# Kernel optimization log

Measured on AMD Instinct MI355X. Metric: run time of the kernel, lower is better.

The kernel has to match this reference:

```python
import jax, jax.numpy as jnp
import numpy as np


def _conv1d_same(seq, w, b):
    # seq: (N, 1, C), w: (1, 1, K) odd K, bias (1,). SAME padding, stride 1.
    k = w.shape[-1]
    p = (k - 1) // 2
    out = jax.lax.conv_general_dilated(
        seq, w, window_strides=(1,), padding=[(p, p)],
        dimension_numbers=("NCH", "OIH", "NCH"))
    return out + b[None, :, None]


def setup_inputs() -> dict:
    key = jax.random.key(0)
    k1, k2, k3 = jax.random.split(key, 3)
    N, C, H, W = 32, 512, 32, 32
    x = jax.random.normal(k1, (N, C, H, W), dtype=jnp.float32)
    wq = jax.random.normal(k2, (1, 1, 5), dtype=jnp.float32) * 0.2
    bq = jax.random.normal(k3, (1,), dtype=jnp.float32) * 0.1
    return {"x": x, "wq": wq, "bq": bq}


def reference(x, wq, bq):
    N, C, H, W = x.shape
    # Global average pool over spatial dims -> (N, 1, C)
    gap = jnp.mean(x, axis=(2, 3)).reshape(N, 1, C)
    # NOTE: original module applies conv_q to BOTH query and key (conv_k unused)
    query = jax.nn.sigmoid(_conv1d_same(gap, wq, bq))          # (N, 1, C)
    key_t = jnp.transpose(query, (0, 2, 1))                    # (N, C, 1)
    # Outer product key @ query -> (N, C, C), softmax over flattened C*C
    qk = jnp.einsum("nci,nij->ncj", key_t, query)              # (N, C, C)
    qk = jax.nn.softmax(qk.reshape(N, C * C), axis=-1).reshape(N, C, C)
    # value: (N, H*W, C)
    value = jnp.transpose(x, (0, 2, 3, 1)).reshape(N, H * W, C)
    att = jnp.einsum("npc,ncd->npd", value, qk)                # (N, HW, C)
    att = jnp.transpose(att, (0, 2, 1)).reshape(N, C, H, W)
    return x * att
```

## Files before the change

kernel.cpp:

```cpp
#include <hip/hip_runtime.h>
#include <math.h>

#define NB 32
#define CC 512
#define HW 1024
#define NJ 10

typedef float vf4 __attribute__((ext_vector_type(4)));

__device__ float g_gap[NB * CC];
__device__ float g_q[NB * CC];
__device__ float g_invZ[NB];

__device__ __forceinline__ float wave_reduce(float s) {
#pragma unroll
  for (int off = 32; off; off >>= 1) s += __shfl_down(s, off, 64);
  return s;
}

__global__ __launch_bounds__(256) void k_gap(const float* __restrict__ x) {
  int wv = threadIdx.x >> 6, lane = threadIdx.x & 63;
  int r0 = blockIdx.x * 16;
#pragma unroll
  for (int it = 0; it < 4; ++it) {
    int row = r0 + wv * 4 + it;
    const float4* xp = (const float4*)x + (size_t)row * 256;
    float s = 0.f;
#pragma unroll
    for (int k = 0; k < 4; ++k) {
      float4 v = xp[lane + 64 * k];
      s += v.x + v.y + v.z + v.w;
    }
    s = wave_reduce(s);
    if (lane == 0) g_gap[row] = s * (1.0f / 1024.0f);
  }
}

__global__ __launch_bounds__(512) void k_q(const float* __restrict__ wq,
                                           const float* __restrict__ bq) {
  int n = blockIdx.x, c = threadIdx.x;
  int wv = c >> 6, lane = c & 63;
  __shared__ float gsh[CC];
  __shared__ float wred[8][NJ];
  const float cj[NJ] = {1.f, 1.f, 0.5f, 1.f / 6.f, 1.f / 24.f, 1.f / 120.f,
                        1.f / 720.f, 1.f / 5040.f, 1.f / 40320.f, 1.f / 362880.f};
  gsh[c] = g_gap[n * CC + c];
  __syncthreads();
  float z = bq[0];
#pragma unroll
  for (int k = 0; k < 5; ++k) {
    int idx = c + k - 2;
    float gv = (idx >= 0 && idx < CC) ? gsh[idx] : 0.f;
    z = fmaf(gv, wq[k], z);
  }
  float qv = 1.f / (1.f + expf(-z));
  g_q[n * CC + c] = qv;
  float pj[NJ];
  float pw = 1.f;
#pragma unroll
  for (int j = 0; j < NJ; ++j) { pj[j] = pw; pw *= qv; }
#pragma unroll
  for (int j = 0; j < NJ; ++j) pj[j] = wave_reduce(pj[j]);
  if (lane == 0) {
#pragma unroll
    for (int j = 0; j < NJ; ++j) wred[wv][j] = pj[j];
  }
  __syncthreads();
  if (c == 0) {
    float Z = 0.f;
#pragma unroll
    for (int j = 0; j < NJ; ++j) {
      float P = 0.f;
#pragma unroll
      for (int w8 = 0; w8 < 8; ++w8) P += wred[w8][j];
      Z = fmaf(cj[j] * P, P, Z);
    }
    g_invZ[n] = 1.f / Z;
  }
}

__global__ __launch_bounds__(512, 2) void k_fused(const float* __restrict__ x,
                                                  float* __restrict__ out) {
  int n = blockIdx.x >> 5, pblk = blockIdx.x & 31;
  int t = threadIdx.x;
  int cg = t >> 3, pg = t & 7;
  int wv = t >> 6, lane = t & 63;

  __shared__ vf4 sred[8][8][NJ + 1];
  __shared__ vf4 sfin[8][NJ + 1];

  const float cj[NJ] = {1.f, 1.f, 0.5f, 1.f / 6.f, 1.f / 24.f, 1.f / 120.f,
                        1.f / 720.f, 1.f / 5040.f, 1.f / 40320.f, 1.f / 362880.f};

  const vf4* x4 = (const vf4*)x;
  size_t base = (size_t)(n * CC + cg * 8) * 256 + (size_t)pblk * 8 + pg;

  vf4 xv[8];
#pragma unroll
  for (int i = 0; i < 8; ++i)
    xv[i] = __builtin_nontemporal_load(&x4[base + (size_t)i * 256]);

  float qv8[8];
  {
    const vf4* q4 = (const vf4*)g_q;
    int qi = (n * CC + cg * 8) >> 2;
    vf4 qa = q4[qi], qb = q4[qi + 1];
    qv8[0] = qa.x; qv8[1] = qa.y; qv8[2] = qa.z; qv8[3] = qa.w;
    qv8[4] = qb.x; qv8[5] = qb.y; qv8[6] = qb.z; qv8[7] = qb.w;
  }
  float invZ = g_invZ[n];

  vf4 acc[NJ];
#pragma unroll
  for (int j = 0; j < NJ; ++j) acc[j] = (vf4){0.f, 0.f, 0.f, 0.f};
#pragma unroll
  for (int i = 0; i < 8; ++i) {
    float qc = qv8[i];
    vf4 v = xv[i];
    float w = 1.f;
#pragma unroll
    for (int j = 0; j < NJ; ++j) {
      acc[j] += v * w;
      w *= qc;
    }
  }
#pragma unroll
  for (int j = 0; j < NJ; ++j) {
#pragma unroll
    for (int m = 8; m <= 32; m <<= 1) {
      acc[j].x += __shfl_xor(acc[j].x, m, 64);
      acc[j].y += __shfl_xor(acc[j].y, m, 64);
      acc[j].z += __shfl_xor(acc[j].z, m, 64);
      acc[j].w += __shfl_xor(acc[j].w, m, 64);
    }
  }
  if (lane < 8) {
#pragma unroll
    for (int j = 0; j < NJ; ++j) sred[wv][lane][j] = acc[j];
  }
  __syncthreads();
  if (t < 80) {
    int pp = t / NJ, j = t - pp * NJ;
    vf4 a = (vf4){0.f, 0.f, 0.f, 0.f};
#pragma unroll
    for (int w8 = 0; w8 < 8; ++w8) a += sred[w8][pp][j];
    sfin[pp][j] = a * (cj[j] * invZ);
  }
  __syncthreads();

  vf4 sj[NJ];
#pragma unroll
  for (int j = 0; j < NJ; ++j) sj[j] = sfin[pg][j];
  vf4* o4 = (vf4*)out;
#pragma unroll
  for (int i = 0; i < 8; ++i) {
    float qd = qv8[i];
    float w = 1.f;
    vf4 att = (vf4){0.f, 0.f, 0.f, 0.f};
#pragma unroll
    for (int j = 0; j < NJ; ++j) {
      att += sj[j] * w;
      w *= qd;
    }
    __builtin_nontemporal_store(xv[i] * att, &o4[base + (size_t)i * 256]);
  }
}

extern "C" void kernel_launch(void* const* d_in, const int* in_sizes, int n_in,
                              void* d_out, int out_size, void* d_ws, size_t ws_size,
                              hipStream_t stream) {
  const float* x  = (const float*)d_in[0];
  const float* wq = (const float*)d_in[1];
  const float* bq = (const float*)d_in[2];
  float* out = (float*)d_out;
  (void)d_ws; (void)ws_size;

  k_gap<<<NB * CC / 16, 256, 0, stream>>>(x);
  k_q<<<NB, 512, 0, stream>>>(wq, bq);
  k_fused<<<NB * 32, 512, 0, stream>>>(x, out);
}
```

Baseline: 143.0 us.

## Widen fused tile to 16 channels by 16 pixel-groups, stage q in shared memory

The fused kernel now has each thread cover 16 channels and each block 64 pixels, which halves the grid to 512 blocks. Per-channel q values are staged in LDS, and the 10-term power accumulation is split into two halves of 5 to limit live registers. Nontemporal loads and stores are swapped for ordinary ones. Each thread now holds 16 x values and the grid is smaller, so register pressure rises and occupancy and parallelism may fall.

Measured after the change: 127.8 us. 1.12x faster.

```diff
diff --git a/kernel.cpp b/kernel.cpp
--- a/kernel.cpp
+++ b/kernel.cpp
@@ -81,65 +81,70 @@
 
 __global__ __launch_bounds__(512, 2) void k_fused(const float* __restrict__ x,
                                                   float* __restrict__ out) {
-  int n = blockIdx.x >> 5, pblk = blockIdx.x & 31;
+  int n = blockIdx.x >> 4, pblk = blockIdx.x & 15;
   int t = threadIdx.x;
-  int cg = t >> 3, pg = t & 7;
+  int cg = t >> 4, pg = t & 15;
   int wv = t >> 6, lane = t & 63;
 
-  __shared__ vf4 sred[8][8][NJ + 1];
-  __shared__ vf4 sfin[8][NJ + 1];
+  __shared__ float qs[CC];
+  __shared__ vf4 sred[8][16][NJ + 1];
+  __shared__ vf4 sfin[16][NJ + 1];
 
   const float cj[NJ] = {1.f, 1.f, 0.5f, 1.f / 6.f, 1.f / 24.f, 1.f / 120.f,
                         1.f / 720.f, 1.f / 5040.f, 1.f / 40320.f, 1.f / 362880.f};
 
   const vf4* x4 = (const vf4*)x;
-  size_t base = (size_t)(n * CC + cg * 8) * 256 + (size_t)pblk * 8 + pg;
+  size_t base = (size_t)(n * CC + cg * 16) * 256 + (size_t)pblk * 16 + pg;
 
-  vf4 xv[8];
+  vf4 xv[16];
 #pragma unroll
-  for (int i = 0; i < 8; ++i)
-    xv[i] = __builtin_nontemporal_load(&x4[base + (size_t)i * 256]);
+  for (int i = 0; i < 16; ++i) xv[i] = x4[base + (size_t)i * 256];
 
-  float qv8[8];
-  {
-    const vf4* q4 = (const vf4*)g_q;
-    int qi = (n * CC + cg * 8) >> 2;
-    vf4 qa = q4[qi], qb = q4[qi + 1];
-    qv8[0] = qa.x; qv8[1] = qa.y; qv8[2] = qa.z; qv8[3] = qa.w;
-    qv8[4] = qb.x; qv8[5] = qb.y; qv8[6] = qb.z; qv8[7] = qb.w;
-  }
+  qs[t] = g_q[n * CC + t];
   float invZ = g_invZ[n];
+  __syncthreads();
 
-  vf4 acc[NJ];
 #pragma unroll
-  for (int j = 0; j < NJ; ++j) acc[j] = (vf4){0.f, 0.f, 0.f, 0.f};
+  for (int half = 0; half < 2; ++half) {
+    vf4 acc[5];
 #pragma unroll
-  for (int i = 0; i < 8; ++i) {
-    float qc = qv8[i];
-    vf4 v = xv[i];
-    float w = 1.f;
+    for (int j = 0; j < 5; ++j) acc[j] = (vf4){0.f, 0.f, 0.f, 0.f};
 #pragma unroll
-    for (int j = 0; j < NJ; ++j) {
-      acc[j] += v * w;
-      w *= qc;
+    for (int i = 0; i < 16; ++i) {
+      float qc = qs[cg * 16 + i];
+      float w;
+      if (half == 0) {
+        w = 1.f;
+      } else {
+        float q2 = qc * qc;
+        float q4 = q2 * q2;
+        w = q4 * qc;
+      }
+      vf4 v = xv[i];
+#pragma unroll
+      for (int j = 0; j < 5; ++j) {
+        acc[j] += v * w;
+        w *= qc;
+      }
+    }
+#pragma unroll
+    for (int j = 0; j < 5; ++j) {
+      acc[j].x += __shfl_xor(acc[j].x, 16, 64);
+      acc[j].y += __shfl_xor(acc[j].y, 16, 64);
+      acc[j].z += __shfl_xor(acc[j].z, 16, 64);
+      acc[j].w += __shfl_xor(acc[j].w, 16, 64);
+      acc[j].x += __shfl_xor(acc[j].x, 32, 64);
+      acc[j].y += __shfl_xor(acc[j].y, 32, 64);
+      acc[j].z += __shfl_xor(acc[j].z, 32, 64);
+      acc[j].w += __shfl_xor(acc[j].w, 32, 64);
+    }
+    if (lane < 16) {
+#pragma unroll
+      for (int j = 0; j < 5; ++j) sred[wv][lane][half * 5 + j] = acc[j];
     }
   }
-#pragma unroll
-  for (int j = 0; j < NJ; ++j) {
-#pragma unroll
-    for (int m = 8; m <= 32; m <<= 1) {
-      acc[j].x += __shfl_xor(acc[j].x, m, 64);
-      acc[j].y += __shfl_xor(acc[j].y, m, 64);
-      acc[j].z += __shfl_xor(acc[j].z, m, 64);
-      acc[j].w += __shfl_xor(acc[j].w, m, 64);
-    }
-  }
-  if (lane < 8) {
-#pragma unroll
-    for (int j = 0; j < NJ; ++j) sred[wv][lane][j] = acc[j];
-  }
   __syncthreads();
-  if (t < 80) {
+  if (t < 160) {
     int pp = t / NJ, j = t - pp * NJ;
     vf4 a = (vf4){0.f, 0.f, 0.f, 0.f};
 #pragma unroll
@@ -153,8 +158,8 @@
   for (int j = 0; j < NJ; ++j) sj[j] = sfin[pg][j];
   vf4* o4 = (vf4*)out;
 #pragma unroll
-  for (int i = 0; i < 8; ++i) {
-    float qd = qv8[i];
+  for (int i = 0; i < 16; ++i) {
+    float qd = qs[cg * 16 + i];
     float w = 1.f;
     vf4 att = (vf4){0.f, 0.f, 0.f, 0.f};
 #pragma unroll
@@ -162,7 +167,7 @@
       att += sj[j] * w;
       w *= qd;
     }
-    __builtin_nontemporal_store(xv[i] * att, &o4[base + (size_t)i * 256]);
+    o4[base + (size_t)i * 256] = xv[i] * att;
   }
 }
 
@@ -177,5 +182,5 @@
 
   k_gap<<<NB * CC / 16, 256, 0, stream>>>(x);
   k_q<<<NB, 512, 0, stream>>>(wq, bq);
-  k_fused<<<NB * 32, 512, 0, stream>>>(x, out);
+  k_fused<<<NB * 16, 512, 0, stream>>>(x, out);
 }
```
